# Kernel tuning notes

Hardware: AMD Instinct MI355X
Metric: run time of the kernel (lower is better)

## Reference

```python
import jax, jax.numpy as jnp
import numpy as np


def _pool_mat(n_in, n_out):
    # AdaptiveAvgPool1d(n_out) over a length-n_in axis, as a dense [n_out, n_in] averaging matrix.
    M = np.zeros((n_out, n_in), dtype=np.float32)
    for i in range(n_out):
        s = (i * n_in) // n_out
        e = -(-((i + 1) * n_in) // n_out)  # ceil
        M[i, s:e] = 1.0 / (e - s)
    return M


def _ln(x, g, b, eps=1e-5):
    m = jnp.mean(x, axis=-1, keepdims=True)
    xc = x - m
    v = jnp.mean(xc * xc, axis=-1, keepdims=True)
    return xc * jax.lax.rsqrt(v + eps) * g + b


def setup_inputs():
    T, TOK, P, N, D, L, C = 16, 16384, 8192, 32768, 128, 8, 16
    key = jax.random.key(0)
    ks = jax.random.split(key, 9)
    x = jax.random.normal(ks[0], (T, TOK, D), dtype=jnp.float32)
    # P node-token positions per timestamp (models padded_node_mask with P True entries)
    node_pos = jnp.sort(jax.vmap(lambda k: jax.random.permutation(k, TOK)[:P])(jax.random.split(ks[1], T)), axis=1).astype(jnp.int32)
    # unique entire-graph node ids per timestamp (scatter destinations)
    node_ids = jax.vmap(lambda k: jax.random.permutation(k, N)[:P])(jax.random.split(ks[2], T)).astype(jnp.int32)
    g_enc = 1.0 + 0.1 * jax.random.normal(ks[3], (D,), dtype=jnp.float32)
    b_enc = 0.1 * jax.random.normal(ks[4], (D,), dtype=jnp.float32)
    g_fin = 1.0 + 0.1 * jax.random.normal(ks[5], (L * C,), dtype=jnp.float32)
    b_fin = 0.1 * jax.random.normal(ks[6], (L * C,), dtype=jnp.float32)
    g_dec = 1.0 + 0.1 * jax.random.normal(ks[7], (C,), dtype=jnp.float32)
    b_dec = 0.1 * jax.random.normal(ks[8], (C,), dtype=jnp.float32)
    return {"x": x, "g_enc": g_enc, "b_enc": b_enc, "g_fin": g_fin, "b_fin": b_fin,
            "g_dec": g_dec, "b_dec": b_dec, "node_pos": node_pos, "node_ids": node_ids,
            "num_nodes": N}


def reference(x, g_enc, b_enc, g_fin, b_fin, g_dec, b_dec, node_pos, node_ids, num_nodes):
    T, TOK, D = x.shape
    C = g_dec.shape[0]
    L = g_fin.shape[0] // C
    N = int(num_nodes)
    # ---- encode ----
    xn = _ln(x, g_enc, b_enc)                                   # encode_layer_norm
    nodes = jnp.take_along_axis(xn, node_pos[:, :, None], axis=1)  # masked gather [T,P,D]
    # _to_entire: scatter node embeddings into zero [T,N,D]
    tee = jnp.zeros((T, N, D), x.dtype).at[jnp.arange(T)[:, None], node_ids].set(nodes)
    A1 = jnp.asarray(_pool_mat(D, C))                            # AdaptiveAvgPool1d(comp_dim)
    pooled = jnp.einsum('tnd,cd->tnc', tee, A1)                  # [T,N,C]
    groups = np.array_split(np.arange(N), L)
    max_len = max(len(g) for g in groups)
    stacked = np.stack([np.pad(g, (0, max_len - len(g))) for g in groups])  # [L,max_len]
    grouped = jnp.take(pooled, jnp.asarray(stacked), axis=1)     # [T,L,max_len,C]
    comp = (grouped.sum(axis=2) / max_len).reshape(T, 1, L * C)  # segment mean-pool
    comp = _ln(comp, g_fin, b_fin)                               # encode_final_layer_norm
    # ---- decode ----
    vals = jnp.broadcast_to(comp.reshape(T, L, 1, C), (T, L, max_len, C)).reshape(T, L * max_len, C)
    tee2 = jnp.zeros((T, N, C), x.dtype).at[:, jnp.asarray(stacked.reshape(-1)), :].set(vals)
    dn = _ln(tee2, g_dec, b_dec)                                 # decode_norm
    A2 = jnp.asarray(_pool_mat(C, D))                            # AdaptiveAvgPool1d(embed_dim)
    out = jnp.einsum('tnc,dc->tnd', dn, A2)                      # [T,N,D]
    return out
```

## Files before the change

kernel.cpp:

```cpp
#include <hip/hip_runtime.h>

#define T_   16
#define TOK_ 16384
#define P_   8192
#define N_   32768
#define D_   128
#define L_   8
#define C_   16

typedef float f32x2 __attribute__((ext_vector_type(2)));
typedef float f32x4 __attribute__((ext_vector_type(4)));

constexpr int K1_BLOCKS     = 2048;
constexpr int BLOCKS_PER_T  = 128;
constexpr int ROWS_PER_WAVE = 16;

__global__ __launch_bounds__(256) void k1_gather_ln_pool(
    const float* __restrict__ x,
    const float* __restrict__ g_enc, const float* __restrict__ b_enc,
    const int* __restrict__ node_pos, const int* __restrict__ node_ids,
    float* __restrict__ partial)
{
    __shared__ float lds[4 * 128];
    const int tid   = threadIdx.x;
    const int lane  = tid & 63;
    const int wid   = tid >> 6;
    const int j     = lane & 15;
    const int q     = lane >> 4;
    const int b     = blockIdx.x;
    const int t     = b >> 7;
    const int chunk = b & 127;
    const int pbase = chunk * 64 + wid * ROWS_PER_WAVE;
    const int tP    = t * P_;
    const float* xt = x + (size_t)t * TOK_ * D_;

    const f32x4 g0  = *(const f32x4*)(g_enc + 8 * j);
    const f32x4 g1  = *(const f32x4*)(g_enc + 8 * j + 4);
    const f32x4 bb0 = *(const f32x4*)(b_enc + 8 * j);
    const f32x4 bb1 = *(const f32x4*)(b_enc + 8 * j + 4);
    const float G = g0.x + g0.y + g0.z + g0.w + g1.x + g1.y + g1.z + g1.w;
    const float B = bb0.x + bb0.y + bb0.z + bb0.w + bb1.x + bb1.y + bb1.z + bb1.w;

    const int posv = node_pos[tP + pbase + j];
    const int nidv = node_ids[tP + pbase + j];

    f32x4 va[4], vb[4];
#pragma unroll
    for (int i = 0; i < 4; ++i) {
        const int p = __shfl(posv, i * 4 + q);
        const float* row = xt + (size_t)p * D_ + 8 * j;
        va[i] = *(const f32x4*)(row);
        vb[i] = *(const f32x4*)(row + 4);
    }

    float acc[L_];
#pragma unroll
    for (int ll = 0; ll < L_; ++ll) acc[ll] = 0.f;

#pragma unroll
    for (int i = 0; i < 4; ++i) {
        const f32x4 a = va[i], c = vb[i];
        float s  = a.x + a.y + a.z + a.w + c.x + c.y + c.z + c.w;
        float ss = a.x*a.x + a.y*a.y + a.z*a.z + a.w*a.w
                 + c.x*c.x + c.y*c.y + c.z*c.z + c.w*c.w;
        float dot = a.x*g0.x + a.y*g0.y + a.z*g0.z + a.w*g0.w
                  + c.x*g1.x + c.y*g1.y + c.z*g1.z + c.w*g1.w;
#pragma unroll
        for (int m = 1; m < 16; m <<= 1) {
            s  += __shfl_xor(s, m);
            ss += __shfl_xor(ss, m);
        }
        const float mean = s * (1.f / 128.f);
        const float rstd = rsqrtf(ss * (1.f / 128.f) - mean * mean + 1e-5f);
        const float srow = (dot - mean * G) * rstd + B;
        const int l = __shfl(nidv, i * 4 + q) >> 12;
#pragma unroll
        for (int ll = 0; ll < L_; ++ll) acc[ll] += (ll == l) ? srow : 0.f;
    }

#pragma unroll
    for (int ll = 0; ll < L_; ++ll) {
        acc[ll] += __shfl_xor(acc[ll], 16);
        acc[ll] += __shfl_xor(acc[ll], 32);
    }
    if (lane < 16) {
#pragma unroll
        for (int ll = 0; ll < L_; ++ll) lds[wid * 128 + ll * 16 + j] = acc[ll];
    }
    __syncthreads();
    if (tid < 128) {
        const float sum = lds[tid] + lds[128 + tid] + lds[256 + tid] + lds[384 + tid];
        partial[(size_t)b * 128 + tid] = sum;
    }
}

__global__ __launch_bounds__(64) void k2_finalize(
    const float* __restrict__ partial,
    const float* __restrict__ g_fin, const float* __restrict__ b_fin,
    const float* __restrict__ g_dec, const float* __restrict__ b_dec,
    float* __restrict__ decoded)
{
    const int t = blockIdx.x;
    const int lane = threadIdx.x;
    const float* pb = partial + (size_t)t * BLOCKS_PER_T * 128;
    float a0 = 0.f, a1 = 0.f;
#pragma unroll 8
    for (int k = 0; k < BLOCKS_PER_T; ++k) {
        a0 += pb[k * 128 + lane];
        a1 += pb[k * 128 + 64 + lane];
    }
    a0 *= (1.f / 32768.f);
    a1 *= (1.f / 32768.f);

    float s = a0 + a1, ss = a0 * a0 + a1 * a1;
#pragma unroll
    for (int m = 1; m < 64; m <<= 1) {
        s  += __shfl_xor(s, m);
        ss += __shfl_xor(ss, m);
    }
    const float mean = s * (1.f / 128.f);
    const float rstd = rsqrtf(ss * (1.f / 128.f) - mean * mean + 1e-5f);
    const float c0 = (a0 - mean) * rstd * g_fin[lane]      + b_fin[lane];
    const float c1 = (a1 - mean) * rstd * g_fin[lane + 64] + b_fin[lane + 64];

    float s0 = c0, q0 = c0 * c0, s1 = c1, q1 = c1 * c1;
#pragma unroll
    for (int m = 1; m < 16; m <<= 1) {
        s0 += __shfl_xor(s0, m); q0 += __shfl_xor(q0, m);
        s1 += __shfl_xor(s1, m); q1 += __shfl_xor(q1, m);
    }
    const float m0 = s0 * (1.f / 16.f), m1 = s1 * (1.f / 16.f);
    const float r0 = rsqrtf(q0 * (1.f / 16.f) - m0 * m0 + 1e-5f);
    const float r1 = rsqrtf(q1 * (1.f / 16.f) - m1 * m1 + 1e-5f);
    const int c = lane & 15;
    const float gd = g_dec[c], bd = b_dec[c];
    decoded[t * 128 + lane]      = (c0 - m0) * r0 * gd + bd;
    decoded[t * 128 + 64 + lane] = (c1 - m1) * r1 * gd + bd;
}

__global__ __launch_bounds__(256) void k3_broadcast(
    const float* __restrict__ decoded, f32x4* __restrict__ out)
{
    const int tid   = threadIdx.x;
    const int b     = blockIdx.x;
    const int t     = b >> 7;
    const int chunk = b & 127;
    const int l     = chunk >> 4;
    const float val = decoded[(t << 7) + (l << 4) + ((tid & 31) >> 1)];
    const f32x4 v4 = {val, val, val, val};
    f32x4* p = out + (((size_t)t << 20) + ((size_t)chunk << 13) + tid);
#pragma unroll
    for (int it = 0; it < 32; ++it)
        p[it << 8] = v4;
}

extern "C" void kernel_launch(void* const* d_in, const int* in_sizes, int n_in,
                              void* d_out, int out_size, void* d_ws, size_t ws_size,
                              hipStream_t stream)
{
    const float* x      = (const float*)d_in[0];
    const float* g_enc  = (const float*)d_in[1];
    const float* b_enc  = (const float*)d_in[2];
    const float* g_fin  = (const float*)d_in[3];
    const float* b_fin  = (const float*)d_in[4];
    const float* g_dec  = (const float*)d_in[5];
    const float* b_dec  = (const float*)d_in[6];
    const int*   node_pos = (const int*)d_in[7];
    const int*   node_ids = (const int*)d_in[8];

    float* partial = (float*)d_ws;
    float* decoded = partial + (size_t)K1_BLOCKS * 128;
    float* out = (float*)d_out;

    hipLaunchKernelGGL(k1_gather_ln_pool, dim3(K1_BLOCKS), dim3(256), 0, stream,
                       x, g_enc, b_enc, node_pos, node_ids, partial);
    hipLaunchKernelGGL(k2_finalize, dim3(T_), dim3(64), 0, stream,
                       partial, g_fin, b_fin, g_dec, b_dec, decoded);
    hipLaunchKernelGGL(k3_broadcast, dim3(2048), dim3(256), 0, stream,
                       decoded, (f32x4*)out);
}
```

Before: 81.11 us.

## Fuse finalize into gather kernel via last-block atomic counter; nontemporal output stores

```diff
diff --git a/kernel.cpp b/kernel.cpp
--- a/kernel.cpp
+++ b/kernel.cpp
@@ -8,20 +8,23 @@
 #define L_   8
 #define C_   16
 
-typedef float f32x2 __attribute__((ext_vector_type(2)));
 typedef float f32x4 __attribute__((ext_vector_type(4)));
 
 constexpr int K1_BLOCKS     = 2048;
 constexpr int BLOCKS_PER_T  = 128;
 constexpr int ROWS_PER_WAVE = 16;
 
-__global__ __launch_bounds__(256) void k1_gather_ln_pool(
+__global__ __launch_bounds__(256) void k1_fused(
     const float* __restrict__ x,
     const float* __restrict__ g_enc, const float* __restrict__ b_enc,
+    const float* __restrict__ g_fin, const float* __restrict__ b_fin,
+    const float* __restrict__ g_dec, const float* __restrict__ b_dec,
     const int* __restrict__ node_pos, const int* __restrict__ node_ids,
-    float* __restrict__ partial)
+    float* __restrict__ partial, float* __restrict__ decoded,
+    int* __restrict__ counters)
 {
     __shared__ float lds[4 * 128];
+    __shared__ int win;
     const int tid   = threadIdx.x;
     const int lane  = tid & 63;
     const int wid   = tid >> 6;
@@ -34,108 +37,116 @@
     const int tP    = t * P_;
     const float* xt = x + (size_t)t * TOK_ * D_;
 
-    const f32x4 g0  = *(const f32x4*)(g_enc + 8 * j);
-    const f32x4 g1  = *(const f32x4*)(g_enc + 8 * j + 4);
-    const f32x4 bb0 = *(const f32x4*)(b_enc + 8 * j);
-    const f32x4 bb1 = *(const f32x4*)(b_enc + 8 * j + 4);
-    const float G = g0.x + g0.y + g0.z + g0.w + g1.x + g1.y + g1.z + g1.w;
-    const float B = bb0.x + bb0.y + bb0.z + bb0.w + bb1.x + bb1.y + bb1.z + bb1.w;
+    {
+        const f32x4 g0  = *(const f32x4*)(g_enc + 8 * j);
+        const f32x4 g1  = *(const f32x4*)(g_enc + 8 * j + 4);
+        const f32x4 bb0 = *(const f32x4*)(b_enc + 8 * j);
+        const f32x4 bb1 = *(const f32x4*)(b_enc + 8 * j + 4);
+        const float G = g0.x + g0.y + g0.z + g0.w + g1.x + g1.y + g1.z + g1.w;
+        const float B = bb0.x + bb0.y + bb0.z + bb0.w + bb1.x + bb1.y + bb1.z + bb1.w;
 
-    const int posv = node_pos[tP + pbase + j];
-    const int nidv = node_ids[tP + pbase + j];
+        const int posv = node_pos[tP + pbase + j];
+        const int nidv = node_ids[tP + pbase + j];
 
-    f32x4 va[4], vb[4];
+        f32x4 va[4], vb[4];
 #pragma unroll
-    for (int i = 0; i < 4; ++i) {
-        const int p = __shfl(posv, i * 4 + q);
-        const float* row = xt + (size_t)p * D_ + 8 * j;
-        va[i] = *(const f32x4*)(row);
-        vb[i] = *(const f32x4*)(row + 4);
+        for (int i = 0; i < 4; ++i) {
+            const int p = __shfl(posv, i * 4 + q);
+            const float* row = xt + (size_t)p * D_ + 8 * j;
+            va[i] = *(const f32x4*)(row);
+            vb[i] = *(const f32x4*)(row + 4);
+        }
+
+        float acc[L_];
+#pragma unroll
+        for (int ll = 0; ll < L_; ++ll) acc[ll] = 0.f;
+
+#pragma unroll
+        for (int i = 0; i < 4; ++i) {
+            const f32x4 a = va[i], c = vb[i];
+            float s  = a.x + a.y + a.z + a.w + c.x + c.y + c.z + c.w;
+            float ss = a.x*a.x + a.y*a.y + a.z*a.z + a.w*a.w
+                     + c.x*c.x + c.y*c.y + c.z*c.z + c.w*c.w;
+            float dot = a.x*g0.x + a.y*g0.y + a.z*g0.z + a.w*g0.w
+                      + c.x*g1.x + c.y*g1.y + c.z*g1.z + c.w*g1.w;
+#pragma unroll
+            for (int m = 1; m < 16; m <<= 1) {
+                s  += __shfl_xor(s, m);
+                ss += __shfl_xor(ss, m);
+            }
+            const float mean = s * (1.f / 128.f);
+            const float rstd = rsqrtf(ss * (1.f / 128.f) - mean * mean + 1e-5f);
+            const float srow = (dot - mean * G) * rstd + B;
+            const int l = __shfl(nidv, i * 4 + q) >> 12;
+#pragma unroll
+            for (int ll = 0; ll < L_; ++ll) acc[ll] += (ll == l) ? srow : 0.f;
+        }
+
+#pragma unroll
+        for (int ll = 0; ll < L_; ++ll) {
+            acc[ll] += __shfl_xor(acc[ll], 16);
+            acc[ll] += __shfl_xor(acc[ll], 32);
+        }
+        if (lane < 16) {
+#pragma unroll
+            for (int ll = 0; ll < L_; ++ll) lds[wid * 128 + ll * 16 + j] = acc[ll];
+        }
+        __syncthreads();
+        if (tid < 128) {
+            const float sum = lds[tid] + lds[128 + tid] + lds[256 + tid] + lds[384 + tid];
+            partial[(size_t)b * 128 + tid] = sum;
+        }
     }
 
-    float acc[L_];
-#pragma unroll
-    for (int ll = 0; ll < L_; ++ll) acc[ll] = 0.f;
-
-#pragma unroll
-    for (int i = 0; i < 4; ++i) {
-        const f32x4 a = va[i], c = vb[i];
-        float s  = a.x + a.y + a.z + a.w + c.x + c.y + c.z + c.w;
-        float ss = a.x*a.x + a.y*a.y + a.z*a.z + a.w*a.w
-                 + c.x*c.x + c.y*c.y + c.z*c.z + c.w*c.w;
-        float dot = a.x*g0.x + a.y*g0.y + a.z*g0.z + a.w*g0.w
-                  + c.x*g1.x + c.y*g1.y + c.z*g1.z + c.w*g1.w;
-#pragma unroll
-        for (int m = 1; m < 16; m <<= 1) {
-            s  += __shfl_xor(s, m);
-            ss += __shfl_xor(ss, m);
-        }
-        const float mean = s * (1.f / 128.f);
-        const float rstd = rsqrtf(ss * (1.f / 128.f) - mean * mean + 1e-5f);
-        const float srow = (dot - mean * G) * rstd + B;
-        const int l = __shfl(nidv, i * 4 + q) >> 12;
-#pragma unroll
-        for (int ll = 0; ll < L_; ++ll) acc[ll] += (ll == l) ? srow : 0.f;
-    }
-
-#pragma unroll
-    for (int ll = 0; ll < L_; ++ll) {
-        acc[ll] += __shfl_xor(acc[ll], 16);
-        acc[ll] += __shfl_xor(acc[ll], 32);
-    }
-    if (lane < 16) {
-#pragma unroll
-        for (int ll = 0; ll < L_; ++ll) lds[wid * 128 + ll * 16 + j] = acc[ll];
+    __threadfence();
+    __syncthreads();
+    if (tid == 0) {
+        const int ret = atomicAdd(&counters[t], 1);
+        win = (ret == BLOCKS_PER_T - 1);
+        __threadfence();
     }
     __syncthreads();
-    if (tid < 128) {
-        const float sum = lds[tid] + lds[128 + tid] + lds[256 + tid] + lds[384 + tid];
-        partial[(size_t)b * 128 + tid] = sum;
+    if (!win) return;
+
+    {
+        const float* pb = partial + (size_t)t * BLOCKS_PER_T * 128;
+        const int ch = tid & 127, h = tid >> 7;
+        float a = 0.f;
+#pragma unroll 8
+        for (int k = 0; k < 64; ++k)
+            a += pb[(h * 64 + k) * 128 + ch];
+        lds[h * 128 + ch] = a;
+        __syncthreads();
+        if (tid < 64) {
+            const int ln = tid;
+            float c0 = (lds[ln] + lds[128 + ln]) * (1.f / 32768.f);
+            float c1 = (lds[64 + ln] + lds[192 + ln]) * (1.f / 32768.f);
+            float s = c0 + c1, ss = c0 * c0 + c1 * c1;
+#pragma unroll
+            for (int m = 1; m < 64; m <<= 1) {
+                s  += __shfl_xor(s, m);
+                ss += __shfl_xor(ss, m);
+            }
+            const float mean = s * (1.f / 128.f);
+            const float rstd = rsqrtf(ss * (1.f / 128.f) - mean * mean + 1e-5f);
+            const float e0 = (c0 - mean) * rstd * g_fin[ln]      + b_fin[ln];
+            const float e1 = (c1 - mean) * rstd * g_fin[ln + 64] + b_fin[ln + 64];
+
+            float s0 = e0, q0 = e0 * e0, s1 = e1, q1 = e1 * e1;
+#pragma unroll
+            for (int m = 1; m < 16; m <<= 1) {
+                s0 += __shfl_xor(s0, m); q0 += __shfl_xor(q0, m);
+                s1 += __shfl_xor(s1, m); q1 += __shfl_xor(q1, m);
+            }
+            const float m0 = s0 * (1.f / 16.f), m1 = s1 * (1.f / 16.f);
+            const float r0 = rsqrtf(q0 * (1.f / 16.f) - m0 * m0 + 1e-5f);
+            const float r1 = rsqrtf(q1 * (1.f / 16.f) - m1 * m1 + 1e-5f);
+            const int c = ln & 15;
+            const float gd = g_dec[c], bd = b_dec[c];
+            decoded[t * 128 + ln]      = (e0 - m0) * r0 * gd + bd;
+            decoded[t * 128 + 64 + ln] = (e1 - m1) * r1 * gd + bd;
+        }
     }
-}
-
-__global__ __launch_bounds__(64) void k2_finalize(
-    const float* __restrict__ partial,
-    const float* __restrict__ g_fin, const float* __restrict__ b_fin,
-    const float* __restrict__ g_dec, const float* __restrict__ b_dec,
-    float* __restrict__ decoded)
-{
-    const int t = blockIdx.x;
-    const int lane = threadIdx.x;
-    const float* pb = partial + (size_t)t * BLOCKS_PER_T * 128;
-    float a0 = 0.f, a1 = 0.f;
-#pragma unroll 8
-    for (int k = 0; k < BLOCKS_PER_T; ++k) {
-        a0 += pb[k * 128 + lane];
-        a1 += pb[k * 128 + 64 + lane];
-    }
-    a0 *= (1.f / 32768.f);
-    a1 *= (1.f / 32768.f);
-
-    float s = a0 + a1, ss = a0 * a0 + a1 * a1;
-#pragma unroll
-    for (int m = 1; m < 64; m <<= 1) {
-        s  += __shfl_xor(s, m);
-        ss += __shfl_xor(ss, m);
-    }
-    const float mean = s * (1.f / 128.f);
-    const float rstd = rsqrtf(ss * (1.f / 128.f) - mean * mean + 1e-5f);
-    const float c0 = (a0 - mean) * rstd * g_fin[lane]      + b_fin[lane];
-    const float c1 = (a1 - mean) * rstd * g_fin[lane + 64] + b_fin[lane + 64];
-
-    float s0 = c0, q0 = c0 * c0, s1 = c1, q1 = c1 * c1;
-#pragma unroll
-    for (int m = 1; m < 16; m <<= 1) {
-        s0 += __shfl_xor(s0, m); q0 += __shfl_xor(q0, m);
-        s1 += __shfl_xor(s1, m); q1 += __shfl_xor(q1, m);
-    }
-    const float m0 = s0 * (1.f / 16.f), m1 = s1 * (1.f / 16.f);
-    const float r0 = rsqrtf(q0 * (1.f / 16.f) - m0 * m0 + 1e-5f);
-    const float r1 = rsqrtf(q1 * (1.f / 16.f) - m1 * m1 + 1e-5f);
-    const int c = lane & 15;
-    const float gd = g_dec[c], bd = b_dec[c];
-    decoded[t * 128 + lane]      = (c0 - m0) * r0 * gd + bd;
-    decoded[t * 128 + 64 + lane] = (c1 - m1) * r1 * gd + bd;
 }
 
 __global__ __launch_bounds__(256) void k3_broadcast(
@@ -151,7 +162,7 @@
     f32x4* p = out + (((size_t)t << 20) + ((size_t)chunk << 13) + tid);
 #pragma unroll
     for (int it = 0; it < 32; ++it)
-        p[it << 8] = v4;
+        __builtin_nontemporal_store(v4, p + (it << 8));
 }
 
 extern "C" void kernel_launch(void* const* d_in, const int* in_sizes, int n_in,
@@ -170,12 +181,13 @@
 
     float* partial = (float*)d_ws;
     float* decoded = partial + (size_t)K1_BLOCKS * 128;
+    int*   counters = (int*)(decoded + T_ * 128);
     float* out = (float*)d_out;
 
-    hipLaunchKernelGGL(k1_gather_ln_pool, dim3(K1_BLOCKS), dim3(256), 0, stream,
-                       x, g_enc, b_enc, node_pos, node_ids, partial);
-    hipLaunchKernelGGL(k2_finalize, dim3(T_), dim3(64), 0, stream,
-                       partial, g_fin, b_fin, g_dec, b_dec, decoded);
+    hipMemsetAsync(counters, 0, T_ * sizeof(int), stream);
+    hipLaunchKernelGGL(k1_fused, dim3(K1_BLOCKS), dim3(256), 0, stream,
+                       x, g_enc, b_enc, g_fin, b_fin, g_dec, b_dec,
+                       node_pos, node_ids, partial, decoded, counters);
     hipLaunchKernelGGL(k3_broadcast, dim3(2048), dim3(256), 0, stream,
                        decoded, (f32x4*)out);
 }
```

New measurement: 304.8 us. +275.7%, slower.
